# Kernel tuning notes

Hardware: AMD Instinct MI355X
Metric: run time of the kernel (lower is better)

## Reference

```python
import jax, jax.numpy as jnp
import numpy as np

UNITS = 256
NUM_HEADS = 8
HEAD_DIM = UNITS // NUM_HEADS
B, N = 8, 2048


def setup_inputs() -> dict:
    key = jax.random.key(0)
    ks = jax.random.split(key, 7)
    node_features = jax.random.normal(ks[0], (B, N, UNITS), dtype=jnp.float32)
    adjacency_matrix = jax.random.randint(ks[1], (B, N, N), 0, 2, dtype=jnp.int32)
    # Glorot-ish scaled dense weights
    s = 1.0 / np.sqrt(UNITS)
    Wq = jax.random.normal(ks[2], (UNITS, UNITS), dtype=jnp.float32) * s
    Wk = jax.random.normal(ks[3], (UNITS, UNITS), dtype=jnp.float32) * s
    Wv = jax.random.normal(ks[4], (UNITS, UNITS), dtype=jnp.float32) * s
    Wo = jax.random.normal(ks[5], (UNITS, UNITS), dtype=jnp.float32) * s
    bo = jnp.zeros((UNITS,), dtype=jnp.float32)
    return {"node_features": node_features, "adjacency_matrix": adjacency_matrix,
            "Wq": Wq, "Wk": Wk, "Wv": Wv, "Wo": Wo, "bo": bo}


def reference(node_features, adjacency_matrix, Wq, Wk, Wv, Wo, bo):
    b, n, _ = node_features.shape
    h, d = NUM_HEADS, HEAD_DIM
    # projections -> [b, h, n, d]
    q = (node_features @ Wq).reshape(b, n, h, d).transpose(0, 2, 1, 3)
    k = (node_features @ Wk).reshape(b, n, h, d).transpose(0, 2, 1, 3)
    v = (node_features @ Wv).reshape(b, n, h, d).transpose(0, 2, 1, 3)
    scores = jnp.einsum('bhqd,bhkd->bhqk', q, k) / jnp.sqrt(jnp.float32(d))
    mask = adjacency_matrix[:, None, :, :] > 0  # [b,1,n,n] broadcasts over heads
    scores = jnp.where(mask, scores, jnp.float32(-1e9))
    w = jax.nn.softmax(scores, axis=-1)
    # dropout is identity at inference (training=None)
    ctx = jnp.einsum('bhqk,bhkd->bhqd', w, v)
    ctx = ctx.transpose(0, 2, 1, 3).reshape(b, n, h * d)
    return ctx @ Wo + bo
```

## Files before the change

### kernel.cpp

```cpp
#include <hip/hip_runtime.h>
#include <cstdint>
#include <cstddef>

#define B_ 8
#define N_ 2048
#define H_ 8
#define D_ 32
#define U_ 256

typedef _Float16 half8 __attribute__((ext_vector_type(8)));
typedef _Float16 half4 __attribute__((ext_vector_type(4)));
typedef float float4v __attribute__((ext_vector_type(4)));

__device__ __forceinline__ float fast_exp2(float x) {
#if __has_builtin(__builtin_amdgcn_exp2f)
  return __builtin_amdgcn_exp2f(x);
#else
  return exp2f(x);
#endif
}

__global__ __launch_bounds__(256, 2)
void k_qkv(const float* __restrict__ X,
           const float* __restrict__ Wq, const float* __restrict__ Wk,
           const float* __restrict__ Wv,
           _Float16* __restrict__ Qg, _Float16* __restrict__ Kg,
           _Float16* __restrict__ VTg)
{
  __shared__ __attribute__((aligned(16))) char qsmem[36864];
  _Float16* Xs = (_Float16*)qsmem;
  _Float16* Ws = (_Float16*)(qsmem + 18432);

  const int tid  = threadIdx.x;
  const int lane = tid & 63;
  const int w    = tid >> 6;
  const int c    = lane & 15;
  const int qd   = lane >> 4;

  const int bx   = blockIdx.x;
  const int proj = bx >> 1;
  const int nh   = bx & 1;
  const int n0l  = nh * 128;
  const int m0   = blockIdx.y * 128;
  const float* Wp = (proj == 0) ? Wq : ((proj == 1) ? Wk : Wv);
  const float wscale = (proj == 0) ? 0.25505413f : 1.0f;

  const float4v zero4 = {0.f, 0.f, 0.f, 0.f};
  float4v acc[2][8];
#pragma unroll
  for (int i = 0; i < 2; ++i)
#pragma unroll
    for (int j = 0; j < 8; ++j) acc[i][j] = zero4;

  for (int kt = 0; kt < 4; ++kt) {
    const int k0 = kt * 64;
    {
      const int row = tid >> 1;
      const int off = (tid & 1) * 32;
      const float* src = X + (size_t)(m0 + row) * U_ + k0 + off;
      _Float16* dst = &Xs[row * 72 + off];
#pragma unroll
      for (int i = 0; i < 4; ++i) {
        float4v a  = *(const float4v*)(src + i * 8);
        float4v b2 = *(const float4v*)(src + i * 8 + 4);
        half8 hv;
        hv[0] = (_Float16)a[0];  hv[1] = (_Float16)a[1];
        hv[2] = (_Float16)a[2];  hv[3] = (_Float16)a[3];
        hv[4] = (_Float16)b2[0]; hv[5] = (_Float16)b2[1];
        hv[6] = (_Float16)b2[2]; hv[7] = (_Float16)b2[3];
        *(half8*)(dst + i * 8) = hv;
      }
    }
    {
      const int kl = tid & 63;
      const int ng = tid >> 6;
      const float* srcw = Wp + (size_t)(k0 + kl) * U_ + n0l + ng * 32;
#pragma unroll
      for (int j = 0; j < 8; ++j) {
        float4v a = *(const float4v*)(srcw + j * 4);
#pragma unroll
        for (int jj = 0; jj < 4; ++jj)
          Ws[(ng * 32 + j * 4 + jj) * 72 + kl] = (_Float16)(a[jj] * wscale);
      }
    }
    __syncthreads();
#pragma unroll
    for (int ks = 0; ks < 2; ++ks) {
      half8 af[2], bf[8];
#pragma unroll
      for (int mt = 0; mt < 2; ++mt)
        af[mt] = *(const half8*)&Xs[(w * 32 + mt * 16 + c) * 72 + ks * 32 + qd * 8];
#pragma unroll
      for (int nt = 0; nt < 8; ++nt)
        bf[nt] = *(const half8*)&Ws[(nt * 16 + c) * 72 + ks * 32 + qd * 8];
#pragma unroll
      for (int mt = 0; mt < 2; ++mt)
#pragma unroll
        for (int nt = 0; nt < 8; ++nt)
          acc[mt][nt] = __builtin_amdgcn_mfma_f32_16x16x32_f16(af[mt], bf[nt], acc[mt][nt], 0, 0, 0);
    }
    __syncthreads();
  }

  const int b   = m0 >> 11;
  const int nb0 = m0 & (N_ - 1);
  if (proj < 2) {
    _Float16* Og = (proj == 0) ? Qg : Kg;
#pragma unroll
    for (int mt = 0; mt < 2; ++mt)
#pragma unroll
      for (int nt = 0; nt < 8; ++nt)
#pragma unroll
        for (int r = 0; r < 4; ++r) {
          const int rowl = w * 32 + mt * 16 + qd * 4 + r;
          Og[(size_t)(b * N_ + nb0 + rowl) * U_ + n0l + nt * 16 + c] = (_Float16)acc[mt][nt][r];
        }
  } else {
    _Float16* tr = (_Float16*)qsmem;
#pragma unroll
    for (int mt = 0; mt < 2; ++mt)
#pragma unroll
      for (int nt = 0; nt < 8; ++nt)
#pragma unroll
        for (int r = 0; r < 4; ++r)
          tr[(nt * 16 + c) * 136 + w * 32 + mt * 16 + qd * 4 + r] = (_Float16)acc[mt][nt][r];
    __syncthreads();
    const int u = tid >> 1;
    const int seg = tid & 1;
    _Float16* dst = VTg + (size_t)(b * U_ + n0l + u) * N_ + nb0 + seg * 64;
#pragma unroll
    for (int i = 0; i < 8; ++i)
      *(half8*)(dst + i * 8) = *(const half8*)&tr[u * 136 + seg * 64 + i * 8];
  }
}

#define KS_H (32 * 264)
#define VT_H (256 * 40)

struct StageRegs {
  half8 k0, k1, v0, v1;
  int a0, a1, a2, a3;
};

__global__ __launch_bounds__(512, 2)
void k_attn(const _Float16* __restrict__ Qg, const _Float16* __restrict__ Kg,
            const _Float16* __restrict__ VTg, const int* __restrict__ Adj,
            _Float16* __restrict__ Cg)
{
  __shared__ __attribute__((aligned(16))) _Float16 KsB[2][KS_H];
  __shared__ __attribute__((aligned(16))) _Float16 VTsB[2][VT_H];
  __shared__ __attribute__((aligned(8)))  unsigned int maskB[2][64];

  const int tid  = threadIdx.x;
  const int lane = tid & 63;
  const int w    = tid >> 6;
  const int c    = lane & 15;
  const int qd   = lane >> 4;
  const int wg   = blockIdx.x;
  const int b    = wg & 7;
  const int q0   = (wg >> 3) * 64;

  const _Float16* kptr = Kg + (size_t)(b * N_ + (tid >> 4)) * U_ + (tid & 15) * 16;
  const _Float16* vptr = VTg + (size_t)(b * U_ + (tid >> 1)) * N_ + (tid & 1) * 16;
  const int rr = lane >> 5;
  const int kk = lane & 31;
  const int* aptr = Adj + (size_t)(b * N_ + q0 + w * 8 + rr) * N_ + kk;

  half8 qb[4];
#pragma unroll
  for (int nt = 0; nt < 4; ++nt)
    qb[nt] = *(const half8*)(Qg + (size_t)(b * N_ + q0 + nt * 16 + c) * U_ + w * D_ + qd * 8);

  const float4v init4 = {-8.f, -8.f, -8.f, -8.f};
  const float4v zero4 = {0.f, 0.f, 0.f, 0.f};
  float4v acc[2][4];
#pragma unroll
  for (int i = 0; i < 2; ++i)
#pragma unroll
    for (int j = 0; j < 4; ++j) acc[i][j] = zero4;
  float lrow[4] = {0.f, 0.f, 0.f, 0.f};

  auto load_tile = [&](int kt) -> StageRegs {
    StageRegs r;
    const _Float16* ks = kptr + (size_t)kt * 32 * U_;
    const _Float16* vs = vptr + (size_t)kt * 32;
    const int* as = aptr + (size_t)kt * 32;
    r.k0 = *(const half8*)ks;  r.k1 = *(const half8*)(ks + 8);
    r.v0 = *(const half8*)vs;  r.v1 = *(const half8*)(vs + 8);
    r.a0 = as[0];
    r.a1 = as[2 * N_];
    r.a2 = as[4 * N_];
    r.a3 = as[6 * N_];
    return r;
  };
  auto store_tile = [&](const StageRegs& r, int buf) {
    _Float16* kd = &KsB[buf][(tid >> 4) * 264 + (tid & 15) * 16];
    *(half8*)kd = r.k0;  *(half8*)(kd + 8) = r.k1;
    _Float16* vd = &VTsB[buf][(tid >> 1) * 40 + (tid & 1) * 16];
    *(half8*)vd = r.v0;  *(half8*)(vd + 8) = r.v1;
    unsigned long long bm;
    bm = __ballot(r.a0 > 0); if (lane == 0) *(unsigned long long*)&maskB[buf][w * 8 + 0] = bm;
    bm = __ballot(r.a1 > 0); if (lane == 0) *(unsigned long long*)&maskB[buf][w * 8 + 2] = bm;
    bm = __ballot(r.a2 > 0); if (lane == 0) *(unsigned long long*)&maskB[buf][w * 8 + 4] = bm;
    bm = __ballot(r.a3 > 0); if (lane == 0) *(unsigned long long*)&maskB[buf][w * 8 + 6] = bm;
  };
  auto compute_tile = [&](int buf) {
    half8 ka0 = *(const half8*)&KsB[buf][(0 * 16 + c) * 264 + w * D_ + qd * 8];
    half8 ka1 = *(const half8*)&KsB[buf][(1 * 16 + c) * 264 + w * D_ + qd * 8];
    half4 va[2][2];
#pragma unroll
    for (int mt = 0; mt < 2; ++mt)
#pragma unroll
      for (int kc = 0; kc < 2; ++kc)
        va[mt][kc] = *(const half4*)&VTsB[buf][(w * D_ + mt * 16 + c) * 40 + kc * 16 + qd * 4];
#pragma unroll
    for (int nt = 0; nt < 4; ++nt) {
      float4v s0 = __builtin_amdgcn_mfma_f32_16x16x32_f16(ka0, qb[nt], init4, 0, 0, 0);
      float4v s1 = __builtin_amdgcn_mfma_f32_16x16x32_f16(ka1, qb[nt], init4, 0, 0, 0);
      const unsigned int mq = maskB[buf][nt * 16 + c];
      const unsigned int t0 = mq >> (qd * 4);
      const unsigned int t1 = mq >> (16 + qd * 4);
      half4 pb0, pb1;
      float ls = 0.f;
#pragma unroll
      for (int r = 0; r < 4; ++r) {
        float e0 = fast_exp2(s0[r]);
        float e1 = fast_exp2(s1[r]);
        float p0 = ((t0 >> r) & 1u) ? e0 : 0.f;
        float p1 = ((t1 >> r) & 1u) ? e1 : 0.f;
        ls += p0 + p1;
        pb0[r] = (_Float16)p0;
        pb1[r] = (_Float16)p1;
      }
      lrow[nt] += ls;
      acc[0][nt] = __builtin_amdgcn_mfma_f32_16x16x16f16(va[0][0], pb0, acc[0][nt], 0, 0, 0);
      acc[0][nt] = __builtin_amdgcn_mfma_f32_16x16x16f16(va[0][1], pb1, acc[0][nt], 0, 0, 0);
      acc[1][nt] = __builtin_amdgcn_mfma_f32_16x16x16f16(va[1][0], pb0, acc[1][nt], 0, 0, 0);
      acc[1][nt] = __builtin_amdgcn_mfma_f32_16x16x16f16(va[1][1], pb1, acc[1][nt], 0, 0, 0);
    }
  };

  {
    StageRegs r = load_tile(0);
    store_tile(r, 0);
  }
  __syncthreads();

#pragma unroll 1
  for (int kt = 0; kt < 64; kt += 2) {
    {
      StageRegs r = load_tile(kt + 1);
      compute_tile(0);
      store_tile(r, 1);
    }
    __syncthreads();
    if (kt + 2 < 64) {
      StageRegs r = load_tile(kt + 2);
      compute_tile(1);
      store_tile(r, 0);
    } else {
      compute_tile(1);
    }
    __syncthreads();
  }

  float rinv[4];
#pragma unroll
  for (int nt = 0; nt < 4; ++nt) {
    float l = lrow[nt];
    l += __shfl_xor(l, 16, 64);
    l += __shfl_xor(l, 32, 64);
    rinv[nt] = (l > 0.f) ? 1.f / l : 0.f;
  }
  _Float16* ctxS = (_Float16*)KsB;
#pragma unroll
  for (int mt = 0; mt < 2; ++mt)
#pragma unroll
    for (int nt = 0; nt < 4; ++nt) {
      half4 hv;
#pragma unroll
      for (int r = 0; r < 4; ++r)
        hv[r] = (_Float16)(acc[mt][nt][r] * rinv[nt]);
      *(half4*)&ctxS[(nt * 16 + c) * 264 + w * D_ + mt * 16 + qd * 4] = hv;
    }
  __syncthreads();
  {
    const int row = tid >> 3;
    const int seg = tid & 7;
    _Float16* dst = Cg + (size_t)(b * N_ + q0 + row) * U_ + seg * 32;
#pragma unroll
    for (int i = 0; i < 4; ++i)
      *(half8*)(dst + i * 8) = *(const half8*)&ctxS[row * 264 + seg * 32 + i * 8];
  }
}

__global__ __launch_bounds__(256, 2)
void k_out(const _Float16* __restrict__ Cg, const float* __restrict__ Wo,
           const float* __restrict__ bo, float* __restrict__ Out)
{
  __shared__ __attribute__((aligned(16))) char osmem[36864];
  _Float16* Xs = (_Float16*)osmem;
  _Float16* Ws = (_Float16*)(osmem + 18432);

  const int tid  = threadIdx.x;
  const int lane = tid & 63;
  const int w    = tid >> 6;
  const int c    = lane & 15;
  const int qd   = lane >> 4;
  const int n0l  = blockIdx.x * 128;
  const int m0   = blockIdx.y * 128;

  const float4v zero4 = {0.f, 0.f, 0.f, 0.f};
  float4v acc[2][8];
#pragma unroll
  for (int i = 0; i < 2; ++i)
#pragma unroll
    for (int j = 0; j < 8; ++j) acc[i][j] = zero4;

  for (int kt = 0; kt < 4; ++kt) {
    const int k0 = kt * 64;
    {
      const int row = tid >> 1;
      const int off = (tid & 1) * 32;
      const _Float16* src = Cg + (size_t)(m0 + row) * U_ + k0 + off;
      _Float16* dst = &Xs[row * 72 + off];
#pragma unroll
      for (int i = 0; i < 4; ++i)
        *(half8*)(dst + i * 8) = *(const half8*)(src + i * 8);
    }
    {
      const int kl = tid & 63;
      const int ng = tid >> 6;
      const float* srcw = Wo + (size_t)(k0 + kl) * U_ + n0l + ng * 32;
#pragma unroll
      for (int j = 0; j < 8; ++j) {
        float4v a = *(const float4v*)(srcw + j * 4);
#pragma unroll
        for (int jj = 0; jj < 4; ++jj)
          Ws[(ng * 32 + j * 4 + jj) * 72 + kl] = (_Float16)a[jj];
      }
    }
    __syncthreads();
#pragma unroll
    for (int ks = 0; ks < 2; ++ks) {
      half8 af[2], bf[8];
#pragma unroll
      for (int mt = 0; mt < 2; ++mt)
        af[mt] = *(const half8*)&Xs[(w * 32 + mt * 16 + c) * 72 + ks * 32 + qd * 8];
#pragma unroll
      for (int nt = 0; nt < 8; ++nt)
        bf[nt] = *(const half8*)&Ws[(nt * 16 + c) * 72 + ks * 32 + qd * 8];
#pragma unroll
      for (int mt = 0; mt < 2; ++mt)
#pragma unroll
        for (int nt = 0; nt < 8; ++nt)
          acc[mt][nt] = __builtin_amdgcn_mfma_f32_16x16x32_f16(af[mt], bf[nt], acc[mt][nt], 0, 0, 0);
    }
    __syncthreads();
  }

#pragma unroll
  for (int nt = 0; nt < 8; ++nt) {
    const float bias = bo[n0l + nt * 16 + c];
#pragma unroll
    for (int mt = 0; mt < 2; ++mt)
#pragma unroll
      for (int r = 0; r < 4; ++r) {
        const int rowl = w * 32 + mt * 16 + qd * 4 + r;
        Out[(size_t)(m0 + rowl) * U_ + n0l + nt * 16 + c] = acc[mt][nt][r] + bias;
      }
  }
}

extern "C" void kernel_launch(void* const* d_in, const int* in_sizes, int n_in,
                              void* d_out, int out_size, void* d_ws, size_t ws_size,
                              hipStream_t stream) {
  const float* X   = (const float*)d_in[0];
  const int*   Adj = (const int*)d_in[1];
  const float* Wq  = (const float*)d_in[2];
  const float* Wk  = (const float*)d_in[3];
  const float* Wv  = (const float*)d_in[4];
  const float* Wo  = (const float*)d_in[5];
  const float* bo  = (const float*)d_in[6];
  float* Out = (float*)d_out;

  const size_t elems = (size_t)B_ * N_ * U_;
  _Float16* Qg  = (_Float16*)d_ws;
  _Float16* Kg  = Qg + elems;
  _Float16* VTg = Kg + elems;
  _Float16* Cg  = VTg + elems;

  k_qkv<<<dim3(6, 128), 256, 0, stream>>>(X, Wq, Wk, Wv, Qg, Kg, VTg);
  k_attn<<<dim3(256), 512, 0, stream>>>(Qg, Kg, VTg, Adj, Cg);
  k_out<<<dim3(2, 128), 256, 0, stream>>>(Cg, Wo, bo, Out);
}
```

Before: 351.2 us.

## Add fp16 pre-conversion kernel, fp16 GEMMs, and 1024-thread attention blocks

Adds a prep kernel that converts X to fp16 and writes transposed fp16 weights (with a Q scale folded in). New QKV and output GEMM kernels load these fp16 operands directly instead of converting fp32 in every tile. The attention kernel now runs 16 waves per block, each covering one head and half of the 64 query rows, with single half8 staging loads per thread and one extra tile prefetched into registers. This adds a kernel launch and workspace traffic, and the 1024-thread blocks limit registers per thread.

```diff
diff --git a/kernel.cpp b/kernel.cpp
--- a/kernel.cpp
+++ b/kernel.cpp
@@ -18,6 +18,153 @@
 #else
   return exp2f(x);
 #endif
+}
+
+__global__ __launch_bounds__(256)
+void k_prep(const float* __restrict__ X,
+            const float* __restrict__ Wq, const float* __restrict__ Wk,
+            const float* __restrict__ Wv, const float* __restrict__ Wo,
+            _Float16* __restrict__ Xh, _Float16* __restrict__ WT)
+{
+  __shared__ __attribute__((aligned(16))) float Ts[64][68];
+  const int tid = threadIdx.x;
+  const int bx = blockIdx.x;
+  if (bx < 4) {
+    const float* W = (bx == 0) ? Wq : (bx == 1) ? Wk : (bx == 2) ? Wv : Wo;
+    const float scale = (bx == 0) ? 0.25505413f : 1.0f;
+    _Float16* dstW = WT + (size_t)bx * (U_ * U_);
+    const int r = tid >> 2, cs = tid & 3;
+    for (int t = 0; t < 16; ++t) {
+      const int k0 = (t >> 2) * 64, n0 = (t & 3) * 64;
+#pragma unroll
+      for (int j = 0; j < 4; ++j)
+        *(float4v*)&Ts[r][cs * 16 + j * 4] =
+            *(const float4v*)(W + (size_t)(k0 + r) * U_ + n0 + cs * 16 + j * 4);
+      __syncthreads();
+#pragma unroll
+      for (int j = 0; j < 4; ++j) {
+        half4 hv;
+#pragma unroll
+        for (int jj = 0; jj < 4; ++jj)
+          hv[jj] = (_Float16)(Ts[cs * 16 + j * 4 + jj][r] * scale);
+        *(half4*)(dstW + (size_t)(n0 + r) * U_ + k0 + cs * 16 + j * 4) = hv;
+      }
+      __syncthreads();
+    }
+  } else {
+    const size_t base = ((size_t)(bx - 4) * 256 + tid) * 32;
+#pragma unroll
+    for (int i = 0; i < 4; ++i) {
+      float4v a  = *(const float4v*)(X + base + i * 8);
+      float4v b2 = *(const float4v*)(X + base + i * 8 + 4);
+      half8 hv;
+      hv[0] = (_Float16)a[0];  hv[1] = (_Float16)a[1];
+      hv[2] = (_Float16)a[2];  hv[3] = (_Float16)a[3];
+      hv[4] = (_Float16)b2[0]; hv[5] = (_Float16)b2[1];
+      hv[6] = (_Float16)b2[2]; hv[7] = (_Float16)b2[3];
+      *(half8*)(Xh + base + i * 8) = hv;
+    }
+  }
+}
+
+__global__ __launch_bounds__(256, 2)
+void k_qkv2(const _Float16* __restrict__ Xh,
+            const _Float16* __restrict__ WTq, const _Float16* __restrict__ WTk,
+            const _Float16* __restrict__ WTv,
+            _Float16* __restrict__ Qg, _Float16* __restrict__ Kg,
+            _Float16* __restrict__ VTg)
+{
+  __shared__ __attribute__((aligned(16))) char qsmem[36864];
+  _Float16* Xs = (_Float16*)qsmem;
+  _Float16* Ws = (_Float16*)(qsmem + 18432);
+
+  const int tid  = threadIdx.x;
+  const int lane = tid & 63;
+  const int w    = tid >> 6;
+  const int c    = lane & 15;
+  const int qd   = lane >> 4;
+
+  const int bx   = blockIdx.x;
+  const int proj = bx >> 1;
+  const int nh   = bx & 1;
+  const int n0l  = nh * 128;
+  const int m0   = blockIdx.y * 128;
+  const _Float16* WT = (proj == 0) ? WTq : ((proj == 1) ? WTk : WTv);
+
+  const float4v zero4 = {0.f, 0.f, 0.f, 0.f};
+  float4v acc[2][8];
+#pragma unroll
+  for (int i = 0; i < 2; ++i)
+#pragma unroll
+    for (int j = 0; j < 8; ++j) acc[i][j] = zero4;
+
+  const int row = tid >> 1;
+  const int off = (tid & 1) * 32;
+  for (int kt = 0; kt < 4; ++kt) {
+    const int k0 = kt * 64;
+    {
+      const _Float16* src = Xh + (size_t)(m0 + row) * U_ + k0 + off;
+      _Float16* dst = &Xs[row * 72 + off];
+#pragma unroll
+      for (int i = 0; i < 4; ++i)
+        *(half8*)(dst + i * 8) = *(const half8*)(src + i * 8);
+    }
+    {
+      const _Float16* srcw = WT + (size_t)(n0l + row) * U_ + k0 + off;
+      _Float16* dstw = &Ws[row * 72 + off];
+#pragma unroll
+      for (int i = 0; i < 4; ++i)
+        *(half8*)(dstw + i * 8) = *(const half8*)(srcw + i * 8);
+    }
+    __syncthreads();
+#pragma unroll
+    for (int ks = 0; ks < 2; ++ks) {
+      half8 af[2], bf[8];
+#pragma unroll
+      for (int mt = 0; mt < 2; ++mt)
+        af[mt] = *(const half8*)&Xs[(w * 32 + mt * 16 + c) * 72 + ks * 32 + qd * 8];
+#pragma unroll
+      for (int nt = 0; nt < 8; ++nt)
+        bf[nt] = *(const half8*)&Ws[(nt * 16 + c) * 72 + ks * 32 + qd * 8];
+#pragma unroll
+      for (int mt = 0; mt < 2; ++mt)
+#pragma unroll
+        for (int nt = 0; nt < 8; ++nt)
+          acc[mt][nt] = __builtin_amdgcn_mfma_f32_16x16x32_f16(af[mt], bf[nt], acc[mt][nt], 0, 0, 0);
+    }
+    __syncthreads();
+  }
+
+  const int b   = m0 >> 11;
+  const int nb0 = m0 & (N_ - 1);
+  if (proj < 2) {
+    _Float16* Og = (proj == 0) ? Qg : Kg;
+#pragma unroll
+    for (int mt = 0; mt < 2; ++mt)
+#pragma unroll
+      for (int nt = 0; nt < 8; ++nt)
+#pragma unroll
+        for (int r = 0; r < 4; ++r) {
+          const int rowl = w * 32 + mt * 16 + qd * 4 + r;
+          Og[(size_t)(b * N_ + nb0 + rowl) * U_ + n0l + nt * 16 + c] = (_Float16)acc[mt][nt][r];
+        }
+  } else {
+    _Float16* tr = (_Float16*)qsmem;
+#pragma unroll
+    for (int mt = 0; mt < 2; ++mt)
+#pragma unroll
+      for (int nt = 0; nt < 8; ++nt)
+#pragma unroll
+        for (int r = 0; r < 4; ++r)
+          tr[(nt * 16 + c) * 136 + w * 32 + mt * 16 + qd * 4 + r] = (_Float16)acc[mt][nt][r];
+    __syncthreads();
+    const int u = tid >> 1;
+    const int seg = tid & 1;
+    _Float16* dst = VTg + (size_t)(b * U_ + n0l + u) * N_ + nb0 + seg * 64;
+#pragma unroll
+    for (int i = 0; i < 8; ++i)
+      *(half8*)(dst + i * 8) = *(const half8*)&tr[u * 136 + seg * 64 + i * 8];
+  }
 }
 
 __global__ __launch_bounds__(256, 2)
@@ -138,11 +285,11 @@
 #define VT_H (256 * 40)
 
 struct StageRegs {
-  half8 k0, k1, v0, v1;
-  int a0, a1, a2, a3;
+  half8 k0, v0;
+  int a0, a1;
 };
 
-__global__ __launch_bounds__(512, 2)
+__global__ __launch_bounds__(1024, 4)
 void k_attn(const _Float16* __restrict__ Qg, const _Float16* __restrict__ Kg,
             const _Float16* __restrict__ VTg, const int* __restrict__ Adj,
             _Float16* __restrict__ Cg)
@@ -154,70 +301,64 @@
   const int tid  = threadIdx.x;
   const int lane = tid & 63;
   const int w    = tid >> 6;
+  const int h    = w & 7;
+  const int qh   = w >> 3;
   const int c    = lane & 15;
   const int qd   = lane >> 4;
   const int wg   = blockIdx.x;
   const int b    = wg & 7;
   const int q0   = (wg >> 3) * 64;
 
-  const _Float16* kptr = Kg + (size_t)(b * N_ + (tid >> 4)) * U_ + (tid & 15) * 16;
-  const _Float16* vptr = VTg + (size_t)(b * U_ + (tid >> 1)) * N_ + (tid & 1) * 16;
+  const _Float16* kptr = Kg + (size_t)(b * N_ + (tid >> 5)) * U_ + (tid & 31) * 8;
+  const _Float16* vptr = VTg + (size_t)(b * U_ + (tid >> 2)) * N_ + (tid & 3) * 8;
   const int rr = lane >> 5;
   const int kk = lane & 31;
-  const int* aptr = Adj + (size_t)(b * N_ + q0 + w * 8 + rr) * N_ + kk;
-
-  half8 qb[4];
-#pragma unroll
-  for (int nt = 0; nt < 4; ++nt)
-    qb[nt] = *(const half8*)(Qg + (size_t)(b * N_ + q0 + nt * 16 + c) * U_ + w * D_ + qd * 8);
+  const int* aptr = Adj + (size_t)(b * N_ + q0 + w * 4 + rr) * N_ + kk;
+
+  half8 qb[2];
+#pragma unroll
+  for (int nt = 0; nt < 2; ++nt)
+    qb[nt] = *(const half8*)(Qg + (size_t)(b * N_ + q0 + qh * 32 + nt * 16 + c) * U_ + h * D_ + qd * 8);
 
   const float4v init4 = {-8.f, -8.f, -8.f, -8.f};
   const float4v zero4 = {0.f, 0.f, 0.f, 0.f};
-  float4v acc[2][4];
+  float4v acc[2][2];
 #pragma unroll
   for (int i = 0; i < 2; ++i)
 #pragma unroll
-    for (int j = 0; j < 4; ++j) acc[i][j] = zero4;
-  float lrow[4] = {0.f, 0.f, 0.f, 0.f};
+    for (int j = 0; j < 2; ++j) acc[i][j] = zero4;
+  float lrow[2] = {0.f, 0.f};
 
   auto load_tile = [&](int kt) -> StageRegs {
     StageRegs r;
-    const _Float16* ks = kptr + (size_t)kt * 32 * U_;
-    const _Float16* vs = vptr + (size_t)kt * 32;
+    r.k0 = *(const half8*)(kptr + (size_t)kt * 32 * U_);
+    r.v0 = *(const half8*)(vptr + (size_t)kt * 32);
     const int* as = aptr + (size_t)kt * 32;
-    r.k0 = *(const half8*)ks;  r.k1 = *(const half8*)(ks + 8);
-    r.v0 = *(const half8*)vs;  r.v1 = *(const half8*)(vs + 8);
     r.a0 = as[0];
     r.a1 = as[2 * N_];
-    r.a2 = as[4 * N_];
-    r.a3 = as[6 * N_];
     return r;
   };
   auto store_tile = [&](const StageRegs& r, int buf) {
-    _Float16* kd = &KsB[buf][(tid >> 4) * 264 + (tid & 15) * 16];
-    *(half8*)kd = r.k0;  *(half8*)(kd + 8) = r.k1;
-    _Float16* vd = &VTsB[buf][(tid >> 1) * 40 + (tid & 1) * 16];
-    *(half8*)vd = r.v0;  *(half8*)(vd + 8) = r.v1;
+    *(half8*)&KsB[buf][(tid >> 5) * 264 + (tid & 31) * 8] = r.k0;
+    *(half8*)&VTsB[buf][(tid >> 2) * 40 + (tid & 3) * 8] = r.v0;
     unsigned long long bm;
-    bm = __ballot(r.a0 > 0); if (lane == 0) *(unsigned long long*)&maskB[buf][w * 8 + 0] = bm;
-    bm = __ballot(r.a1 > 0); if (lane == 0) *(unsigned long long*)&maskB[buf][w * 8 + 2] = bm;
-    bm = __ballot(r.a2 > 0); if (lane == 0) *(unsigned long long*)&maskB[buf][w * 8 + 4] = bm;
-    bm = __ballot(r.a3 > 0); if (lane == 0) *(unsigned long long*)&maskB[buf][w * 8 + 6] = bm;
+    bm = __ballot(r.a0 > 0); if (lane == 0) *(unsigned long long*)&maskB[buf][w * 4 + 0] = bm;
+    bm = __ballot(r.a1 > 0); if (lane == 0) *(unsigned long long*)&maskB[buf][w * 4 + 2] = bm;
   };
   auto compute_tile = [&](int buf) {
-    half8 ka0 = *(const half8*)&KsB[buf][(0 * 16 + c) * 264 + w * D_ + qd * 8];
-    half8 ka1 = *(const half8*)&KsB[buf][(1 * 16 + c) * 264 + w * D_ + qd * 8];
+    half8 ka0 = *(const half8*)&KsB[buf][(0 * 16 + c) * 264 + h * D_ + qd * 8];
+    half8 ka1 = *(const half8*)&KsB[buf][(1 * 16 + c) * 264 + h * D_ + qd * 8];
     half4 va[2][2];
 #pragma unroll
     for (int mt = 0; mt < 2; ++mt)
 #pragma unroll
       for (int kc = 0; kc < 2; ++kc)
-        va[mt][kc] = *(const half4*)&VTsB[buf][(w * D_ + mt * 16 + c) * 40 + kc * 16 + qd * 4];
-#pragma unroll
-    for (int nt = 0; nt < 4; ++nt) {
+        va[mt][kc] = *(const half4*)&VTsB[buf][(h * D_ + mt * 16 + c) * 40 + kc * 16 + qd * 4];
+#pragma unroll
+    for (int nt = 0; nt < 2; ++nt) {
       float4v s0 = __builtin_amdgcn_mfma_f32_16x16x32_f16(ka0, qb[nt], init4, 0, 0, 0);
       float4v s1 = __builtin_amdgcn_mfma_f32_16x16x32_f16(ka1, qb[nt], init4, 0, 0, 0);
-      const unsigned int mq = maskB[buf][nt * 16 + c];
+      const unsigned int mq = maskB[buf][qh * 32 + nt * 16 + c];
       const unsigned int t0 = mq >> (qd * 4);
       const unsigned int t1 = mq >> (16 + qd * 4);
       half4 pb0, pb1;
@@ -240,33 +381,26 @@
     }
   };
 
-  {
-    StageRegs r = load_tile(0);
-    store_tile(r, 0);
-  }
+  StageRegs rA = load_tile(0);
+  store_tile(rA, 0);
+  StageRegs rB = load_tile(1);
   __syncthreads();
 
 #pragma unroll 1
   for (int kt = 0; kt < 64; kt += 2) {
-    {
-      StageRegs r = load_tile(kt + 1);
-      compute_tile(0);
-      store_tile(r, 1);
-    }
-    __syncthreads();
-    if (kt + 2 < 64) {
-      StageRegs r = load_tile(kt + 2);
-      compute_tile(1);
-      store_tile(r, 0);
-    } else {
-      compute_tile(1);
-    }
-    __syncthreads();
-  }
-
-  float rinv[4];
-#pragma unroll
-  for (int nt = 0; nt < 4; ++nt) {
+    if (kt + 2 < 64) rA = load_tile(kt + 2);
+    compute_tile(0);
+    store_tile(rB, 1);
+    __syncthreads();
+    if (kt + 3 < 64) rB = load_tile(kt + 3);
+    compute_tile(1);
+    if (kt + 2 < 64) store_tile(rA, 0);
+    __syncthreads();
+  }
+
+  float rinv[2];
+#pragma unroll
+  for (int nt = 0; nt < 2; ++nt) {
     float l = lrow[nt];
     l += __shfl_xor(l, 16, 64);
     l += __shfl_xor(l, 32, 64);
@@ -276,21 +410,93 @@
 #pragma unroll
   for (int mt = 0; mt < 2; ++mt)
 #pragma unroll
-    for (int nt = 0; nt < 4; ++nt) {
+    for (int nt = 0; nt < 2; ++nt) {
       half4 hv;
 #pragma unroll
       for (int r = 0; r < 4; ++r)
         hv[r] = (_Float16)(acc[mt][nt][r] * rinv[nt]);
-      *(half4*)&ctxS[(nt * 16 + c) * 264 + w * D_ + mt * 16 + qd * 4] = hv;
+      *(half4*)&ctxS[(qh * 32 + nt * 16 + c) * 264 + h * D_ + mt * 16 + qd * 4] = hv;
     }
   __syncthreads();
   {
-    const int row = tid >> 3;
-    const int seg = tid & 7;
-    _Float16* dst = Cg + (size_t)(b * N_ + q0 + row) * U_ + seg * 32;
-#pragma unroll
-    for (int i = 0; i < 4; ++i)
-      *(half8*)(dst + i * 8) = *(const half8*)&ctxS[row * 264 + seg * 32 + i * 8];
+    const int row = tid >> 4;
+    const int seg = tid & 15;
+    _Float16* dst = Cg + (size_t)(b * N_ + q0 + row) * U_ + seg * 16;
+    *(half8*)(dst + 0) = *(const half8*)&ctxS[row * 264 + seg * 16];
+    *(half8*)(dst + 8) = *(const half8*)&ctxS[row * 264 + seg * 16 + 8];
+  }
+}
+
+__global__ __launch_bounds__(256, 2)
+void k_out2(const _Float16* __restrict__ Cg, const _Float16* __restrict__ WTo,
+            const float* __restrict__ bo, float* __restrict__ Out)
+{
+  __shared__ __attribute__((aligned(16))) char osmem[36864];
+  _Float16* Xs = (_Float16*)osmem;
+  _Float16* Ws = (_Float16*)(osmem + 18432);
+
+  const int tid  = threadIdx.x;
+  const int lane = tid & 63;
+  const int w    = tid >> 6;
+  const int c    = lane & 15;
+  const int qd   = lane >> 4;
+  const int n0l  = blockIdx.x * 128;
+  const int m0   = blockIdx.y * 128;
+
+  const float4v zero4 = {0.f, 0.f, 0.f, 0.f};
+  float4v acc[2][8];
+#pragma unroll
+  for (int i = 0; i < 2; ++i)
+#pragma unroll
+    for (int j = 0; j < 8; ++j) acc[i][j] = zero4;
+
+  const int row = tid >> 1;
+  const int off = (tid & 1) * 32;
+  for (int kt = 0; kt < 4; ++kt) {
+    const int k0 = kt * 64;
+    {
+      const _Float16* src = Cg + (size_t)(m0 + row) * U_ + k0 + off;
+      _Float16* dst = &Xs[row * 72 + off];
+#pragma unroll
+      for (int i = 0; i < 4; ++i)
+        *(half8*)(dst + i * 8) = *(const half8*)(src + i * 8);
+    }
+    {
+      const _Float16* srcw = WTo + (size_t)(n0l + row) * U_ + k0 + off;
+      _Float16* dstw = &Ws[row * 72 + off];
+#pragma unroll
+      for (int i = 0; i < 4; ++i)
+        *(half8*)(dstw + i * 8) = *(const half8*)(srcw + i * 8);
+    }
+    __syncthreads();
+#pragma unroll
+    for (int ks = 0; ks < 2; ++ks) {
+      half8 af[2], bf[8];
+#pragma unroll
+      for (int mt = 0; mt < 2; ++mt)
+        af[mt] = *(const half8*)&Xs[(w * 32 + mt * 16 + c) * 72 + ks * 32 + qd * 8];
+#pragma unroll
+      for (int nt = 0; nt < 8; ++nt)
+        bf[nt] = *(const half8*)&Ws[(nt * 16 + c) * 72 + ks * 32 + qd * 8];
+#pragma unroll
+      for (int mt = 0; mt < 2; ++mt)
+#pragma unroll
+        for (int nt = 0; nt < 8; ++nt)
+          acc[mt][nt] = __builtin_amdgcn_mfma_f32_16x16x32_f16(af[mt], bf[nt], acc[mt][nt], 0, 0, 0);
+    }
+    __syncthreads();
+  }
+
+#pragma unroll
+  for (int nt = 0; nt < 8; ++nt) {
+    const float bias = bo[n0l + nt * 16 + c];
+#pragma unroll
+    for (int mt = 0; mt < 2; ++mt)
+#pragma unroll
+      for (int r = 0; r < 4; ++r) {
+        const int rowl = w * 32 + mt * 16 + qd * 4 + r;
+        Out[(size_t)(m0 + rowl) * U_ + n0l + nt * 16 + c] = acc[mt][nt][r] + bias;
+      }
   }
 }
 
@@ -385,12 +591,31 @@
   float* Out = (float*)d_out;
 
   const size_t elems = (size_t)B_ * N_ * U_;
-  _Float16* Qg  = (_Float16*)d_ws;
-  _Float16* Kg  = Qg + elems;
-  _Float16* VTg = Kg + elems;
-  _Float16* Cg  = VTg + elems;
-
-  k_qkv<<<dim3(6, 128), 256, 0, stream>>>(X, Wq, Wk, Wv, Qg, Kg, VTg);
-  k_attn<<<dim3(256), 512, 0, stream>>>(Qg, Kg, VTg, Adj, Cg);
-  k_out<<<dim3(2, 128), 256, 0, stream>>>(Cg, Wo, bo, Out);
-}
+  const size_t need  = (4 * elems + 4 * (size_t)(U_ * U_)) * sizeof(_Float16);
+
+  if (ws_size >= need) {
+    _Float16* A   = (_Float16*)d_ws;
+    _Float16* Qg  = A + elems;
+    _Float16* Kg  = Qg + elems;
+    _Float16* VTg = Kg + elems;
+    _Float16* WT  = VTg + elems;
+    _Float16* WTq = WT;
+    _Float16* WTk = WT + (size_t)U_ * U_;
+    _Float16* WTv = WT + 2 * (size_t)U_ * U_;
+    _Float16* WTo = WT + 3 * (size_t)U_ * U_;
+
+    k_prep<<<dim3(516), 256, 0, stream>>>(X, Wq, Wk, Wv, Wo, A, WT);
+    k_qkv2<<<dim3(6, 128), 256, 0, stream>>>(A, WTq, WTk, WTv, Qg, Kg, VTg);
+    k_attn<<<dim3(256), 1024, 0, stream>>>(Qg, Kg, VTg, Adj, A );
+    k_out2<<<dim3(2, 128), 256, 0, stream>>>(A , WTo, bo, Out);
+  } else {
+    _Float16* Qg  = (_Float16*)d_ws;
+    _Float16* Kg  = Qg + elems;
+    _Float16* VTg = Kg + elems;
+    _Float16* Cg  = VTg + elems;
+
+    k_qkv<<<dim3(6, 128), 256, 0, stream>>>(X, Wq, Wk, Wv, Qg, Kg, VTg);
+    k_attn<<<dim3(256), 1024, 0, stream>>>(Qg, Kg, VTg, Adj, Cg);
+    k_out<<<dim3(2, 128), 256, 0, stream>>>(Cg, Wo, bo, Out);
+  }
+}
```

New measurement: 339.6 us. 3.3% less time.
